# Optimization experiments

Measured on AMD Instinct MI355X. Metric: run time of the kernel, lower is better.

## Reference

```python
import jax, jax.numpy as jnp
import numpy as np

N = 131072      # total nodes
E = 262144      # directed edges (~2 per node, molecular graphs)
B = 4096        # number of graphs
D = 300         # emb_dim
L = 5           # num_layer
MAXN = 96       # max nodes per graph (static cap)
NUM_ATOM, NUM_CHI = 120, 3
NUM_BOND, NUM_DIR = 6, 3   # bond type vocab incl. self-loop id 4; bond direction
BN_EPS = 1e-5
SELF_LOOP_BOND = 4


def setup_inputs() -> dict:
    key = jax.random.key(0)
    ks = jax.random.split(key, 24)
    s = 1.0 / np.sqrt(D)
    x = jnp.stack([jax.random.randint(ks[0], (N,), 0, NUM_ATOM),
                   jax.random.randint(ks[1], (N,), 0, NUM_CHI)], axis=1)
    edge_index = jax.random.randint(ks[2], (2, E), 0, N)
    edge_attr = jnp.stack([jax.random.randint(ks[3], (E,), 0, 4),
                           jax.random.randint(ks[4], (E,), 0, NUM_DIR)], axis=1)
    batch = jnp.sort(jax.random.randint(ks[5], (N,), 0, B)).at[-1].set(B - 1)
    return dict(
        x=x, edge_index=edge_index, edge_attr=edge_attr, batch=batch, max_nodes=MAXN,
        atom_emb1=jax.random.normal(ks[6], (NUM_ATOM, D)) * s,
        atom_emb2=jax.random.normal(ks[7], (NUM_CHI, D)) * s,
        edge_emb1=jax.random.normal(ks[8], (L, NUM_BOND, D)) * s,
        edge_emb2=jax.random.normal(ks[9], (L, NUM_DIR, D)) * s,
        W1=jax.random.normal(ks[10], (L, D, 2 * D)) * s,
        b1=jnp.zeros((L, 2 * D)),
        W2=jax.random.normal(ks[11], (L, 2 * D, D)) * (1.0 / np.sqrt(2 * D)),
        b2=jnp.zeros((L, D)),
        bn_gamma=jax.random.uniform(ks[12], (L, D), minval=0.8, maxval=1.2),
        bn_beta=jax.random.normal(ks[13], (L, D)) * 0.05,
        bn_mean=jax.random.normal(ks[14], (L, D)) * 0.05,
        bn_var=jax.random.uniform(ks[15], (L, D), minval=0.5, maxval=1.5),
    )


def reference(x, edge_index, edge_attr, batch, max_nodes,
              atom_emb1, atom_emb2, edge_emb1, edge_emb2,
              W1, b1, W2, b2, bn_gamma, bn_beta, bn_mean, bn_var):
    n = x.shape[0]
    # add self-loops with edge_attr [SELF_LOOP_BOND, 0] (chem GIN convention)
    loops = jnp.arange(n, dtype=edge_index.dtype)
    src = jnp.concatenate([edge_index[0], loops])
    dst = jnp.concatenate([edge_index[1], loops])
    sl = jnp.stack([jnp.full((n,), SELF_LOOP_BOND, edge_attr.dtype),
                    jnp.zeros((n,), edge_attr.dtype)], axis=1)
    ea = jnp.concatenate([edge_attr, sl], axis=0)

    h = atom_emb1[x[:, 0]] + atom_emb2[x[:, 1]]  # [N, D]
    for l in range(L):
        e = edge_emb1[l][ea[:, 0]] + edge_emb2[l][ea[:, 1]]     # [E+N, D]
        msg = h[src] + e                                         # gather + add
        agg = jax.ops.segment_sum(msg, dst, num_segments=n)      # scatter-add
        h = jnp.maximum(agg @ W1[l] + b1[l], 0.0) @ W2[l] + b2[l]  # GIN MLP
        h = bn_gamma[l] * (h - bn_mean[l]) * jax.lax.rsqrt(bn_var[l] + BN_EPS) + bn_beta[l]
        if l < L - 1:
            h = jnp.maximum(h, 0.0)

    # ragged -> dense pack (replaces the per-graph python copy loop)
    counts = jax.ops.segment_sum(jnp.ones((n,), jnp.int32), batch, num_segments=B)
    offsets = jnp.concatenate([jnp.zeros((1,), counts.dtype), jnp.cumsum(counts)[:-1]])
    pos = jnp.arange(n, dtype=counts.dtype) - offsets[batch]     # within-graph index
    padded = jnp.zeros((B, max_nodes, h.shape[1]), h.dtype).at[batch, pos].set(h)
    padding_mask = jnp.arange(max_nodes)[None, :] >= counts[:, None]
    return padded, padding_mask
```

## Files before the change

kernel.cpp:

```cpp
#include <hip/hip_runtime.h>

typedef _Float16 f16;
typedef __attribute__((ext_vector_type(8))) _Float16 f16x8;
typedef __attribute__((ext_vector_type(4))) _Float16 f16x4;
typedef __attribute__((ext_vector_type(4))) float f32x4;

#define D_      300
#define DP      320
#define L_      5
#define MAXN_   96
#define NGRAPH  4096
#define MAXDEG  32

__global__ void k_prep_w(const float* __restrict__ W1, const float* __restrict__ W2,
                         f16* __restrict__ W1t, f16* __restrict__ W2t) {
  const int T1 = L_ * 640 * 320;
  const int T2 = L_ * 304 * 640;
  for (int idx = blockIdx.x * blockDim.x + threadIdx.x; idx < T1 + T2;
       idx += gridDim.x * blockDim.x) {
    if (idx < T1) {
      int l = idx / (640 * 320), r = idx % (640 * 320);
      int j = r / 320, k = r % 320;
      W1t[idx] = (j < 600 && k < 300) ? (f16)W1[(l * 300 + k) * 600 + j] : (f16)0.0f;
    } else {
      int i2 = idx - T1;
      int l = i2 / (304 * 640), r = i2 % (304 * 640);
      int c = r / 640, k = r % 640;
      W2t[i2] = (c < 300 && k < 600) ? (f16)W2[(l * 600 + k) * 300 + c] : (f16)0.0f;
    }
  }
}

__global__ void k_prep_eemb(const float* __restrict__ ee1, const float* __restrict__ ee2,
                            float* __restrict__ eemb) {
  int total = L_ * 13 * 304;
  for (int idx = blockIdx.x * blockDim.x + threadIdx.x; idx < total;
       idx += gridDim.x * blockDim.x) {
    int l = idx / (13 * 304), r = idx % (13 * 304);
    int c = r / 304, d = r % 304;
    int bond = (c == 12) ? 4 : (c / 3);
    int dir  = (c == 12) ? 0 : (c % 3);
    eemb[idx] = (d < 300) ? ee1[(l * 6 + bond) * 300 + d] + ee2[(l * 3 + dir) * 300 + d]
                          : 0.0f;
  }
}

__global__ void k_bc_init(int* counts, int* offsets) {
  int i = blockIdx.x * blockDim.x + threadIdx.x;
  if (i < NGRAPH) { counts[i] = 0; offsets[i] = 0x7fffffff; }
}
__global__ void k_zero_i32(int* p, int n) {
  for (int i = blockIdx.x * blockDim.x + threadIdx.x; i < n; i += gridDim.x * blockDim.x)
    p[i] = 0;
}
__global__ void k_bc_count(const int* __restrict__ batch, int n, int* counts, int* offsets) {
  int i = blockIdx.x * blockDim.x + threadIdx.x;
  if (i < n) { int b = batch[i]; atomicAdd(&counts[b], 1); atomicMin(&offsets[b], i); }
}
__global__ void k_pos(const int* __restrict__ batch, const int* __restrict__ offsets,
                      int n, int* __restrict__ pos) {
  int i = blockIdx.x * blockDim.x + threadIdx.x;
  if (i < n) pos[i] = i - offsets[batch[i]];
}
__global__ void k_mask(const int* __restrict__ counts, float* __restrict__ mask) {
  int i = blockIdx.x * blockDim.x + threadIdx.x;
  if (i < NGRAPH * MAXN_) {
    int b = i / MAXN_, j = i % MAXN_;
    mask[i] = (j >= counts[b]) ? 1.0f : 0.0f;
  }
}
__global__ void k_zero(uint4* __restrict__ p, long nchunks) {
  for (long i = blockIdx.x * (long)blockDim.x + threadIdx.x; i < nchunks;
       i += (long)gridDim.x * blockDim.x)
    p[i] = make_uint4(0u, 0u, 0u, 0u);
}

__global__ void k_epack(const int* __restrict__ src, const int* __restrict__ dst,
                        const int* __restrict__ ea, int ne,
                        int* __restrict__ deg, int* __restrict__ epack) {
  int e = blockIdx.x * blockDim.x + threadIdx.x;
  if (e < ne) {
    int t = dst[e];
    int p = atomicAdd(&deg[t], 1);
    if (p < MAXDEG) epack[t * MAXDEG + p] = src[e] | ((ea[2 * e] * 3 + ea[2 * e + 1]) << 17);
  }
}

__global__ void k_init_h(const int* __restrict__ x, const float* __restrict__ ae1,
                         const float* __restrict__ ae2, f16* __restrict__ h, int n) {
  long total = (long)n * DP;
  for (long idx = blockIdx.x * (long)blockDim.x + threadIdx.x; idx < total;
       idx += (long)gridDim.x * blockDim.x) {
    int i = idx / DP, d = idx % DP;
    if (d < 300) {
      int a1 = x[2 * i], a2 = x[2 * i + 1];
      h[idx] = (f16)(ae1[a1 * 300 + d] + ae2[a2 * 300 + d]);
    } else h[idx] = (f16)0.0f;
  }
}

__launch_bounds__(512)
__global__ void k_gather(const f16* __restrict__ hin, f16* __restrict__ agg,
                         const int* __restrict__ deg, const int* __restrict__ epack,
                         const float* __restrict__ em, int n) {
  int w = threadIdx.x >> 6, lane = threadIdx.x & 63;
  int node = blockIdx.x * 8 + w;
  if (node >= n) return;
  float acc[5];
  const float* ems = em + 12 * 304;
#pragma unroll
  for (int k = 0; k < 5; k++) {
    int d = lane + 64 * k;
    acc[k] = (d < 300) ? (float)hin[node * DP + d] + ems[d] : 0.0f;
  }
  int dg = deg[node]; if (dg > MAXDEG) dg = MAXDEG;
  for (int j = 0; j < dg; j++) {
    int v = epack[node * MAXDEG + j];
    int s = v & 0x1FFFF, c = v >> 17;
    const f16* hr = hin + s * DP;
    const float* er = em + c * 304;
#pragma unroll
    for (int k = 0; k < 5; k++) {
      int d = lane + 64 * k;
      if (d < 300) acc[k] += (float)hr[d] + er[d];
    }
  }
#pragma unroll
  for (int k = 0; k < 5; k++) {
    int d = lane + 64 * k;
    agg[node * DP + d] = (f16)((d < 300) ? acc[k] : 0.0f);
  }
}

template<int LAST>
__launch_bounds__(512)
__global__ void k_mlp(const f16* agg,
                      f16* hout,
                      const f16* __restrict__ W1t,
                      const f16* __restrict__ W2t,
                      const float* __restrict__ b1, const float* __restrict__ b2,
                      const float* __restrict__ bng, const float* __restrict__ bnb,
                      const float* __restrict__ bnm, const float* __restrict__ bnv,
                      float* __restrict__ outp, const int* __restrict__ batch,
                      const int* __restrict__ pos) {
  __shared__ __align__(16) unsigned char smem[122880];
  f16* As = (f16*)smem;
  f16* Hs = (f16*)(smem + 40960);
  f16* Os = (f16*)smem;

  const int tid = threadIdx.x, w = tid >> 6, lane = tid & 63;
  const int lr = lane & 15, lk = lane >> 4;
  const int n0 = blockIdx.x * 64;

#pragma unroll
  for (int q = 0; q < 5; q++) {
    int c = q * 512 + tid;
    int row = c / 40, cc = c % 40;
    f16x8 v = *(const f16x8*)(agg + (size_t)(n0 + row) * DP + cc * 8);
    *(f16x8*)(As + row * 320 + ((cc ^ (row & 7)) << 3)) = v;
  }
  __syncthreads();

  {
    const f16* wbase = W1t + (size_t)(w * 16 + lr) * 320 + lk * 8;
    f16x8 bcur[10], bnxt[10];
#pragma unroll
    for (int ks = 0; ks < 10; ks++) bcur[ks] = *(const f16x8*)(wbase + ks * 32);
#pragma unroll
    for (int j = 0; j < 5; j++) {
      const int col = (w + 8 * j) * 16 + lr;
      if (j < 4) {
        const f16* wb2 = wbase + (size_t)(j + 1) * 128 * 320;
#pragma unroll
        for (int ks = 0; ks < 10; ks++) bnxt[ks] = *(const f16x8*)(wb2 + ks * 32);
      }
      f32x4 a1[4] = {};
#pragma unroll
      for (int ks = 0; ks < 10; ks++) {
        int kc = ks * 4 + lk;
#pragma unroll
        for (int rg = 0; rg < 4; rg++) {
          int row = rg * 16 + lr;
          f16x8 af = *(const f16x8*)(As + row * 320 + ((kc ^ (row & 7)) << 3));
          a1[rg] = __builtin_amdgcn_mfma_f32_16x16x32_f16(af, bcur[ks], a1[rg], 0, 0, 0);
        }
      }
      float bv = (col < 600) ? b1[col] : 0.0f;
      int chq = col >> 3, cof = col & 7;
#pragma unroll
      for (int rg = 0; rg < 4; rg++)
#pragma unroll
        for (int i = 0; i < 4; i++) {
          int row = rg * 16 + lk * 4 + i;
          Hs[row * 640 + (((chq ^ (row & 7)) << 3) | cof)] =
              (f16)fmaxf(a1[rg][i] + bv, 0.0f);
        }
#pragma unroll
      for (int ks = 0; ks < 10; ks++) bcur[ks] = bnxt[ks];
    }
  }
  __syncthreads();

  {
    const f16* w2b[4];
#pragma unroll
    for (int j = 0; j < 3; j++) {
      int ct = w + 8 * j; if (ct > 18) ct = 18;
      w2b[j] = W2t + (size_t)(ct * 16 + lr) * 640 + lk * 8;
    }
    w2b[3] = w2b[2];
    f16x8 bA[10], bB[10];
#pragma unroll
    for (int ks = 0; ks < 10; ks++) bA[ks] = *(const f16x8*)(w2b[0] + ks * 32);
#pragma unroll
    for (int j = 0; j < 3; j++) {
      const int ct = w + 8 * j;
      if (ct < 19) {
        const int col = ct * 16 + lr;
#pragma unroll
        for (int ks = 0; ks < 10; ks++) bB[ks] = *(const f16x8*)(w2b[j] + 320 + ks * 32);
        f32x4 c2[4] = {};
#pragma unroll
        for (int ks = 0; ks < 10; ks++) {
          int kc = ks * 4 + lk;
#pragma unroll
          for (int rg = 0; rg < 4; rg++) {
            int row = rg * 16 + lr;
            f16x8 hf = *(const f16x8*)(Hs + row * 640 + ((kc ^ (row & 7)) << 3));
            c2[rg] = __builtin_amdgcn_mfma_f32_16x16x32_f16(hf, bA[ks], c2[rg], 0, 0, 0);
          }
        }
        if (j < 2) {
#pragma unroll
          for (int ks = 0; ks < 10; ks++) bA[ks] = *(const f16x8*)(w2b[j + 1] + ks * 32);
        }
#pragma unroll
        for (int ks = 10; ks < 20; ks++) {
          int kc = ks * 4 + lk;
#pragma unroll
          for (int rg = 0; rg < 4; rg++) {
            int row = rg * 16 + lr;
            f16x8 hf = *(const f16x8*)(Hs + row * 640 + ((kc ^ (row & 7)) << 3));
            c2[rg] = __builtin_amdgcn_mfma_f32_16x16x32_f16(hf, bB[ks - 10], c2[rg], 0, 0, 0);
          }
        }
        bool real = col < 300;
        float b2v = real ? b2[col] : 0.0f;
        float sc  = real ? bng[col] * rsqrtf(bnv[col] + 1e-5f) : 0.0f;
        float mu  = real ? bnm[col] : 0.0f;
        float be  = real ? bnb[col] : 0.0f;
        int chq = col >> 3, cof = col & 7;
#pragma unroll
        for (int rg = 0; rg < 4; rg++)
#pragma unroll
          for (int i = 0; i < 4; i++) {
            int row = rg * 16 + lk * 4 + i;
            float v = (c2[rg][i] + b2v - mu) * sc + be;
            if (!LAST) v = fmaxf(v, 0.0f);
            Os[row * 320 + (((chq ^ (row & 7)) << 3) | cof)] =
                real ? (f16)v : (f16)0.0f;
          }
      }
    }
  }

  if (tid < 128) {
    int row = tid >> 1, cc = 38 + (tid & 1);
    f16x8 zz = {};
    *(f16x8*)(Os + row * 320 + ((cc ^ (row & 7)) << 3)) = zz;
  }
  __syncthreads();

  if (!LAST) {
#pragma unroll
    for (int q = 0; q < 5; q++) {
      int c = q * 512 + tid;
      int row = c / 40, cc = c % 40;
      *(f16x8*)(hout + (size_t)(n0 + row) * DP + cc * 8) =
          *(const f16x8*)(Os + row * 320 + ((cc ^ (row & 7)) << 3));
    }
  } else {
    for (int idx = tid; idx < 64 * 75; idx += 512) {
      int row = idx / 75, c4 = idx % 75;
      int node = n0 + row;
      int g = batch[node], p = pos[node];
      if (p < MAXN_) {
        int col = c4 * 4;
        const f16* s = Os + row * 320 + (((col >> 3) ^ (row & 7)) << 3) + (col & 7);
        f16x4 hv = *(const f16x4*)s;
        float4 v = make_float4((float)hv[0], (float)hv[1], (float)hv[2], (float)hv[3]);
        *(float4*)(outp + ((long)g * MAXN_ + p) * 300 + col) = v;
      }
    }
  }
}

extern "C" void kernel_launch(void* const* d_in, const int* in_sizes, int n_in,
                              void* d_out, int out_size, void* d_ws, size_t ws_size,
                              hipStream_t stream) {
  const int* x     = (const int*)d_in[0];
  const int* ei    = (const int*)d_in[1];
  const int* ea    = (const int*)d_in[2];
  const int* batch = (const int*)d_in[3];
  const float* ae1 = (const float*)d_in[5];
  const float* ae2 = (const float*)d_in[6];
  const float* ee1 = (const float*)d_in[7];
  const float* ee2 = (const float*)d_in[8];
  const float* W1  = (const float*)d_in[9];
  const float* b1  = (const float*)d_in[10];
  const float* W2  = (const float*)d_in[11];
  const float* b2  = (const float*)d_in[12];
  const float* bng = (const float*)d_in[13];
  const float* bnb = (const float*)d_in[14];
  const float* bnm = (const float*)d_in[15];
  const float* bnv = (const float*)d_in[16];

  const int N = in_sizes[3];
  const int E = in_sizes[2] / 2;

  char* ws = (char*)d_ws;
  f16*   hX    = (f16*)ws;
  f16*   hY    = (f16*)(ws + 83886080);
  f16*   W1t   = (f16*)(ws + 167772160);
  f16*   W2t   = (f16*)(ws + 169820160);
  float* eemb  = (float*)(ws + 171765760);
  int*   epack = (int*)(ws + 171844800);
  int*   deg   = (int*)(ws + 188622016);
  int*   pos   = (int*)(ws + 189146304);
  int*   counts= (int*)(ws + 189670592);
  int*   offs  = (int*)(ws + 189686976);

  float* outp  = (float*)d_out;
  float* maskp = outp + (long)NGRAPH * MAXN_ * D_;

  hipLaunchKernelGGL(k_prep_w, dim3(2048), dim3(256), 0, stream, W1, W2, W1t, W2t);
  hipLaunchKernelGGL(k_prep_eemb, dim3(80), dim3(256), 0, stream, ee1, ee2, eemb);
  hipLaunchKernelGGL(k_bc_init, dim3(16), dim3(256), 0, stream, counts, offs);
  hipLaunchKernelGGL(k_zero_i32, dim3(512), dim3(256), 0, stream, deg, N);
  hipLaunchKernelGGL(k_bc_count, dim3((N + 255) / 256), dim3(256), 0, stream, batch, N, counts, offs);
  hipLaunchKernelGGL(k_pos, dim3((N + 255) / 256), dim3(256), 0, stream, batch, offs, N, pos);
  hipLaunchKernelGGL(k_mask, dim3((NGRAPH * MAXN_ + 255) / 256), dim3(256), 0, stream, counts, maskp);
  hipLaunchKernelGGL(k_epack, dim3((E + 255) / 256), dim3(256), 0, stream,
                     ei, ei + E, ea, E, deg, epack);
  hipLaunchKernelGGL(k_zero, dim3(4096), dim3(256), 0, stream,
                     (uint4*)outp, (long)NGRAPH * MAXN_ * D_ / 4);
  hipLaunchKernelGGL(k_init_h, dim3(8192), dim3(256), 0, stream, x, ae1, ae2, hX, N);

  for (int l = 0; l < L_; l++) {
    const f16* hi = (l & 1) ? hY : hX;
    f16*       ag = (l & 1) ? hX : hY;
    hipLaunchKernelGGL(k_gather, dim3(N / 8), dim3(512), 0, stream,
                       hi, ag, deg, epack, eemb + l * 13 * 304, N);
    if (l < L_ - 1)
      hipLaunchKernelGGL((k_mlp<0>), dim3(N / 64), dim3(512), 0, stream,
                         ag, ag,
                         W1t + l * 640 * 320, W2t + l * 304 * 640,
                         b1 + l * 600, b2 + l * 300,
                         bng + l * 300, bnb + l * 300, bnm + l * 300, bnv + l * 300,
                         outp, batch, pos);
    else
      hipLaunchKernelGGL((k_mlp<1>), dim3(N / 64), dim3(512), 0, stream,
                         ag, ag,
                         W1t + l * 640 * 320, W2t + l * 304 * 640,
                         b1 + l * 600, b2 + l * 300,
                         bng + l * 300, bnb + l * 300, bnm + l * 300, bnv + l * 300,
                         outp, batch, pos);
  }
}
```

Before: 1.759 ms.

## Reorder MLP GEMM loops to k-outer so A fragments are reused across column tiles

```diff
diff --git a/kernel.cpp b/kernel.cpp
--- a/kernel.cpp
+++ b/kernel.cpp
@@ -163,28 +163,36 @@
 
   {
     const f16* wbase = W1t + (size_t)(w * 16 + lr) * 320 + lk * 8;
-    f16x8 bcur[10], bnxt[10];
-#pragma unroll
-    for (int ks = 0; ks < 10; ks++) bcur[ks] = *(const f16x8*)(wbase + ks * 32);
+    f32x4 a1[5][4] = {};
+    f16x8 bcur[5], bnxt[5];
+#pragma unroll
+    for (int j = 0; j < 5; j++)
+      bcur[j] = *(const f16x8*)(wbase + (size_t)j * 40960);
+#pragma unroll
+    for (int ks = 0; ks < 10; ks++) {
+      if (ks < 9) {
+#pragma unroll
+        for (int j = 0; j < 5; j++)
+          bnxt[j] = *(const f16x8*)(wbase + (size_t)j * 40960 + (ks + 1) * 32);
+      }
+      int kc = ks * 4 + lk;
+      f16x8 af[4];
+#pragma unroll
+      for (int rg = 0; rg < 4; rg++) {
+        int row = rg * 16 + lr;
+        af[rg] = *(const f16x8*)(As + row * 320 + ((kc ^ (row & 7)) << 3));
+      }
+#pragma unroll
+      for (int j = 0; j < 5; j++)
+#pragma unroll
+        for (int rg = 0; rg < 4; rg++)
+          a1[j][rg] = __builtin_amdgcn_mfma_f32_16x16x32_f16(af[rg], bcur[j], a1[j][rg], 0, 0, 0);
+#pragma unroll
+      for (int j = 0; j < 5; j++) bcur[j] = bnxt[j];
+    }
 #pragma unroll
     for (int j = 0; j < 5; j++) {
       const int col = (w + 8 * j) * 16 + lr;
-      if (j < 4) {
-        const f16* wb2 = wbase + (size_t)(j + 1) * 128 * 320;
-#pragma unroll
-        for (int ks = 0; ks < 10; ks++) bnxt[ks] = *(const f16x8*)(wb2 + ks * 32);
-      }
-      f32x4 a1[4] = {};
-#pragma unroll
-      for (int ks = 0; ks < 10; ks++) {
-        int kc = ks * 4 + lk;
-#pragma unroll
-        for (int rg = 0; rg < 4; rg++) {
-          int row = rg * 16 + lr;
-          f16x8 af = *(const f16x8*)(As + row * 320 + ((kc ^ (row & 7)) << 3));
-          a1[rg] = __builtin_amdgcn_mfma_f32_16x16x32_f16(af, bcur[ks], a1[rg], 0, 0, 0);
-        }
-      }
       float bv = (col < 600) ? b1[col] : 0.0f;
       int chq = col >> 3, cof = col & 7;
 #pragma unroll
@@ -193,57 +201,50 @@
         for (int i = 0; i < 4; i++) {
           int row = rg * 16 + lk * 4 + i;
           Hs[row * 640 + (((chq ^ (row & 7)) << 3) | cof)] =
-              (f16)fmaxf(a1[rg][i] + bv, 0.0f);
+              (f16)fmaxf(a1[j][rg][i] + bv, 0.0f);
         }
-#pragma unroll
-      for (int ks = 0; ks < 10; ks++) bcur[ks] = bnxt[ks];
     }
   }
   __syncthreads();
 
   {
-    const f16* w2b[4];
+    const f16* w2b[3];
 #pragma unroll
     for (int j = 0; j < 3; j++) {
       int ct = w + 8 * j; if (ct > 18) ct = 18;
       w2b[j] = W2t + (size_t)(ct * 16 + lr) * 640 + lk * 8;
     }
-    w2b[3] = w2b[2];
-    f16x8 bA[10], bB[10];
-#pragma unroll
-    for (int ks = 0; ks < 10; ks++) bA[ks] = *(const f16x8*)(w2b[0] + ks * 32);
+    f32x4 c2[3][4] = {};
+    f16x8 bcur[3], bnxt[3];
+#pragma unroll
+    for (int j = 0; j < 3; j++) bcur[j] = *(const f16x8*)(w2b[j]);
+#pragma unroll
+    for (int ks = 0; ks < 20; ks++) {
+      if (ks < 19) {
+#pragma unroll
+        for (int j = 0; j < 3; j++)
+          bnxt[j] = *(const f16x8*)(w2b[j] + (ks + 1) * 32);
+      }
+      int kc = ks * 4 + lk;
+      f16x8 hf[4];
+#pragma unroll
+      for (int rg = 0; rg < 4; rg++) {
+        int row = rg * 16 + lr;
+        hf[rg] = *(const f16x8*)(Hs + row * 640 + ((kc ^ (row & 7)) << 3));
+      }
+#pragma unroll
+      for (int j = 0; j < 3; j++)
+#pragma unroll
+        for (int rg = 0; rg < 4; rg++)
+          c2[j][rg] = __builtin_amdgcn_mfma_f32_16x16x32_f16(hf[rg], bcur[j], c2[j][rg], 0, 0, 0);
+#pragma unroll
+      for (int j = 0; j < 3; j++) bcur[j] = bnxt[j];
+    }
 #pragma unroll
     for (int j = 0; j < 3; j++) {
       const int ct = w + 8 * j;
       if (ct < 19) {
         const int col = ct * 16 + lr;
-#pragma unroll
-        for (int ks = 0; ks < 10; ks++) bB[ks] = *(const f16x8*)(w2b[j] + 320 + ks * 32);
-        f32x4 c2[4] = {};
-#pragma unroll
-        for (int ks = 0; ks < 10; ks++) {
-          int kc = ks * 4 + lk;
-#pragma unroll
-          for (int rg = 0; rg < 4; rg++) {
-            int row = rg * 16 + lr;
-            f16x8 hf = *(const f16x8*)(Hs + row * 640 + ((kc ^ (row & 7)) << 3));
-            c2[rg] = __builtin_amdgcn_mfma_f32_16x16x32_f16(hf, bA[ks], c2[rg], 0, 0, 0);
-          }
-        }
-        if (j < 2) {
-#pragma unroll
-          for (int ks = 0; ks < 10; ks++) bA[ks] = *(const f16x8*)(w2b[j + 1] + ks * 32);
-        }
-#pragma unroll
-        for (int ks = 10; ks < 20; ks++) {
-          int kc = ks * 4 + lk;
-#pragma unroll
-          for (int rg = 0; rg < 4; rg++) {
-            int row = rg * 16 + lr;
-            f16x8 hf = *(const f16x8*)(Hs + row * 640 + ((kc ^ (row & 7)) << 3));
-            c2[rg] = __builtin_amdgcn_mfma_f32_16x16x32_f16(hf, bB[ks - 10], c2[rg], 0, 0, 0);
-          }
-        }
         bool real = col < 300;
         float b2v = real ? b2[col] : 0.0f;
         float sc  = real ? bng[col] * rsqrtf(bnv[col] + 1e-5f) : 0.0f;
@@ -255,7 +256,7 @@
 #pragma unroll
           for (int i = 0; i < 4; i++) {
             int row = rg * 16 + lk * 4 + i;
-            float v = (c2[rg][i] + b2v - mu) * sc + be;
+            float v = (c2[j][rg][i] + b2v - mu) * sc + be;
             if (!LAST) v = fmaxf(v, 0.0f);
             Os[row * 320 + (((chq ^ (row & 7)) << 3) | cof)] =
                 real ? (f16)v : (f16)0.0f;
```

Result: slower. 1.910 ms (+8.6%).
